# Optimization experiments

Measured on AMD Instinct MI355X. Metric: run time of the kernel, lower is better.

## Reference

```python
import jax, jax.numpy as jnp
import numpy as np

V = 100000   # num_vertices
E = 3200000  # directed edges (symmetric: both directions of E//2 undirected edges)
B = 8        # batch of meshes
C = 3        # xyz vertex features


def setup_inputs() -> dict:
    key = jax.random.key(0)
    k1, k2, k3, k4 = jax.random.split(key, 4)
    src = jax.random.randint(k1, (E // 2,), 0, V, dtype=jnp.int32)
    dst = jax.random.randint(k2, (E // 2,), 0, V, dtype=jnp.int32)
    edge_index = jnp.stack([jnp.concatenate([src, dst]),
                            jnp.concatenate([dst, src])])  # (2, E)
    features = jax.random.normal(k3, (B, V, C), dtype=jnp.float32)
    target_features = jax.random.normal(k4, (B, V, C), dtype=jnp.float32)
    return {"features": features, "target_features": target_features,
            "edge_index": edge_index}


def _sym_laplacian(edge_index, num_nodes, dtype):
    """get_laplacian(..., normalization='sym'): L = I - D^{-1/2} A D^{-1/2}.
    Returns (lap_row, lap_col, lap_weight) as edge list with self-loops appended."""
    row, col = edge_index
    ones = jnp.ones(row.shape, dtype)
    deg = jax.ops.segment_sum(ones, row, num_segments=num_nodes)
    deg_inv_sqrt = jnp.where(deg > 0, deg, 1.0) ** -0.5
    deg_inv_sqrt = jnp.where(deg > 0, deg_inv_sqrt, 0.0)
    ew = -deg_inv_sqrt[row] * deg_inv_sqrt[col]
    loop = jnp.arange(num_nodes, dtype=row.dtype)
    lap_row = jnp.concatenate([row, loop])
    lap_col = jnp.concatenate([col, loop])
    lap_w = jnp.concatenate([ew, jnp.ones((num_nodes,), dtype)])
    return lap_row, lap_col, lap_w


def _apply_laplacian(x, lap_row, lap_col, lap_w, num_nodes):
    # x: (B, V, C) -> gather on source vertex, scale, scatter_add on target vertex
    xt = jnp.swapaxes(x, 0, 1)                       # (V, B, C)
    msg = xt[lap_row] * lap_w[:, None, None]          # (E+V, B, C)
    out = jax.ops.segment_sum(msg, lap_col, num_segments=num_nodes)  # (V, B, C)
    return jnp.swapaxes(out, 0, 1)                    # (B, V, C)


def reference(features, target_features, edge_index):
    lap_row, lap_col, lap_w = _sym_laplacian(edge_index, V, features.dtype)
    lap_x = _apply_laplacian(features, lap_row, lap_col, lap_w, V)
    lap_y = _apply_laplacian(target_features, lap_row, lap_col, lap_w, V)
    # per-batch mse averaged over batch == global mean since shapes are uniform
    return jnp.mean((lap_x - lap_y) ** 2)
```

## Files before the change

### kernel.cpp

```cpp
#include <hip/hip_runtime.h>

#define C_CONST 3
#define B_CONST 8
#define BC 24
#define NCH 3
#define VP 196
#define NP 512
#define CAP 6784
#define K1_T 512
#define K1_EPT 16
#define K1_EPB (K1_T * K1_EPT)
#define PREP_T 512
#define GT 256

typedef float floatx2 __attribute__((ext_vector_type(2)));

__global__ __launch_bounds__(K1_T) void bucket_kernel(
    const int* __restrict__ row, const int* __restrict__ col, int E,
    int* __restrict__ pcount, unsigned int* __restrict__ bucket)
{
    __shared__ unsigned int sl[K1_EPB];
    __shared__ int hist[NP];
    __shared__ int offs[NP];
    __shared__ int gbase[NP];
    __shared__ int scanbuf[NP];
    int tid = threadIdx.x;
    for (int i = tid; i < NP; i += K1_T) hist[i] = 0;
    __syncthreads();

    int e0 = blockIdx.x * K1_EPB + tid * K1_EPT;
    unsigned int pk[K1_EPT];
    int pe[K1_EPT];
    int rk[K1_EPT];
    if (e0 + K1_EPT <= E) {
        int rs[K1_EPT], cs[K1_EPT];
#pragma unroll
        for (int q = 0; q < K1_EPT / 4; q++) {
            int4 rv = *(const int4*)(row + e0 + q * 4);
            int4 cv = *(const int4*)(col + e0 + q * 4);
            rs[q*4+0] = rv.x; rs[q*4+1] = rv.y; rs[q*4+2] = rv.z; rs[q*4+3] = rv.w;
            cs[q*4+0] = cv.x; cs[q*4+1] = cv.y; cs[q*4+2] = cv.z; cs[q*4+3] = cv.w;
        }
#pragma unroll
        for (int i = 0; i < K1_EPT; i++) {
            int c = cs[i];
            int p = c / VP;
            pe[i] = p;
            pk[i] = (unsigned int)rs[i] | ((unsigned int)(c - p * VP) << 17);
        }
    } else {
#pragma unroll
        for (int i = 0; i < K1_EPT; i++) {
            int e = e0 + i;
            if (e < E) {
                int c = col[e];
                int p = c / VP;
                pe[i] = p;
                pk[i] = (unsigned int)row[e] | ((unsigned int)(c - p * VP) << 17);
            } else { pe[i] = -1; pk[i] = 0; }
        }
    }
#pragma unroll
    for (int i = 0; i < K1_EPT; i++)
        rk[i] = (pe[i] >= 0) ? atomicAdd(&hist[pe[i]], 1) : 0;
    __syncthreads();

    scanbuf[tid] = hist[tid];
    __syncthreads();
    for (int off = 1; off < NP; off <<= 1) {
        int t2 = (tid >= off) ? scanbuf[tid - off] : 0;
        __syncthreads();
        scanbuf[tid] += t2;
        __syncthreads();
    }
    offs[tid] = scanbuf[tid] - hist[tid];
    gbase[tid] = (hist[tid] > 0) ? atomicAdd(&pcount[tid], hist[tid]) : 0;
    __syncthreads();

#pragma unroll
    for (int i = 0; i < K1_EPT; i++)
        if (pe[i] >= 0) sl[offs[pe[i]] + rk[i]] = pk[i];
    __syncthreads();

    int wid = tid >> 6, lane = tid & 63;
    for (int pp = wid; pp < NP; pp += K1_T / 64) {
        int cnt = hist[pp];
        int lo = offs[pp];
        int gb = gbase[pp];
        unsigned int* dst = bucket + (size_t)pp * CAP;
        for (int i = lane; i < cnt; i += 64) {
            int pos = gb + i;
            if (pos < CAP) dst[pos] = sl[lo + i];
        }
    }
}

__global__ __launch_bounds__(PREP_T) void prep_sort_kernel(
    const int* __restrict__ pcount, unsigned int* __restrict__ bucket,
    const float* __restrict__ x, const float* __restrict__ y, int V,
    int* __restrict__ rowstart, int* __restrict__ degs,
    unsigned char* __restrict__ wh)
{
    __shared__ unsigned int sorted[CAP];
    __shared__ int rowptr[VP + 1];
    __shared__ int cur[VP];
    __shared__ int scanbuf[256];
    __shared__ float ssc[VP];
    __shared__ unsigned char tile[VP * BC];
    int p = blockIdx.x;
    int tid = threadIdx.x;
    int n = pcount[p]; if (n > CAP) n = CAP;
    unsigned int* bp = bucket + (size_t)p * CAP;

    for (int i = tid; i < VP; i += PREP_T) cur[i] = 0;
    __syncthreads();
    for (int i = tid; i < n; i += PREP_T) atomicAdd(&cur[bp[i] >> 17], 1);
    __syncthreads();

    if (tid < 256) scanbuf[tid] = (tid < VP) ? cur[tid] : 0;
    __syncthreads();
    for (int off = 1; off < 256; off <<= 1) {
        int t2 = 0;
        if (tid < 256 && tid >= off) t2 = scanbuf[tid - off];
        __syncthreads();
        if (tid < 256) scanbuf[tid] += t2;
        __syncthreads();
    }
    if (tid == 0) rowptr[0] = 0;
    if (tid < VP) rowptr[tid + 1] = scanbuf[tid];
    for (int i = tid; i < VP; i += PREP_T) cur[i] = 0;
    __syncthreads();

    for (int i = tid; i < n; i += PREP_T) {
        unsigned int e = bp[i];
        int cl = e >> 17;
        int slot = rowptr[cl] + atomicAdd(&cur[cl], 1);
        sorted[slot] = e & 0x1FFFFu;
    }
    __syncthreads();

    for (int i = tid; i < n; i += PREP_T) bp[i] = sorted[i];

    int vb = p * VP;
    int nv = V - vb; if (nv > VP) nv = VP; if (nv < 0) nv = 0;
    for (int i = tid; i < nv; i += PREP_T) {
        int dg = rowptr[i + 1] - rowptr[i];
        rowstart[vb + i] = p * CAP + rowptr[i];
        degs[vb + i] = dg;
        ssc[i] = (dg > 0) ? rsqrtf((float)dg) : 1.0f;
    }
    __syncthreads();

    int ns = nv * C_CONST;
    int ns4 = ns >> 2;
    for (int idx = tid; idx < B_CONST * ns4; idx += PREP_T) {
        int b = idx / ns4;
        int q = idx - b * ns4;
        size_t off = ((size_t)b * V + vb) * C_CONST + (size_t)q * 4;
        float4 xv = *(const float4*)(x + off);
        float4 yv = *(const float4*)(y + off);
        float vals[4] = {xv.x - yv.x, xv.y - yv.y, xv.z - yv.z, xv.w - yv.w};
        int f0 = q * 4;
#pragma unroll
        for (int j = 0; j < 4; j++) {
            int f = f0 + j;
            int vl = f / C_CONST;
            int c = f - vl * C_CONST;
            float w = ssc[vl] * vals[j];
            int packed = __builtin_amdgcn_cvt_pk_fp8_f32(w, w, 0, false);
            tile[vl * BC + b * C_CONST + c] = (unsigned char)(packed & 0xFF);
        }
    }
    __syncthreads();

    int nbytes = nv * BC;
    uint4* dst = (uint4*)(wh + (size_t)vb * BC);
    const uint4* srcT = (const uint4*)tile;
    for (int i = tid; i < (nbytes >> 4); i += PREP_T) dst[i] = srcT[i];
}

__global__ __launch_bounds__(GT) void gather_loss_kernel(
    const unsigned int* __restrict__ sorted, const int* __restrict__ rowstart,
    const int* __restrict__ degs, const uint2* __restrict__ whp,
    int V, float inv_n, float* __restrict__ out)
{
    __shared__ float ls[GT / 64];
    int item = blockIdx.x * GT + threadIdx.x;
    float s = 0.0f;
    if (item < V * NCH) {
        int v = item / NCH;
        int j = item - v * NCH;
        int q0 = rowstart[v];
        int dg = degs[v];
        float a0=0.f,a1=0.f,a2=0.f,a3=0.f,a4=0.f,a5=0.f,a6=0.f,a7=0.f;
        for (int q = q0; q < q0 + dg; q++) {
            int r = (int)sorted[q];
            uint2 u = whp[r * NCH + j];
            floatx2 f0 = __builtin_amdgcn_cvt_pk_f32_fp8((int)u.x, false);
            floatx2 f1 = __builtin_amdgcn_cvt_pk_f32_fp8((int)u.x, true);
            floatx2 f2 = __builtin_amdgcn_cvt_pk_f32_fp8((int)u.y, false);
            floatx2 f3 = __builtin_amdgcn_cvt_pk_f32_fp8((int)u.y, true);
            a0 += f0.x; a1 += f0.y; a2 += f1.x; a3 += f1.y;
            a4 += f2.x; a5 += f2.y; a6 += f3.x; a7 += f3.y;
        }
        float dvv = (dg > 0) ? rsqrtf((float)dg) : 0.0f;
        float di  = (dg > 0) ? sqrtf((float)dg)  : 1.0f;
        uint2 su = whp[v * NCH + j];
        floatx2 s0 = __builtin_amdgcn_cvt_pk_f32_fp8((int)su.x, false);
        floatx2 s1 = __builtin_amdgcn_cvt_pk_f32_fp8((int)su.x, true);
        floatx2 s2 = __builtin_amdgcn_cvt_pk_f32_fp8((int)su.y, false);
        floatx2 s3 = __builtin_amdgcn_cvt_pk_f32_fp8((int)su.y, true);
        float r0 = s0.x * di - dvv * a0;
        float r1 = s0.y * di - dvv * a1;
        float r2 = s1.x * di - dvv * a2;
        float r3 = s1.y * di - dvv * a3;
        float r4 = s2.x * di - dvv * a4;
        float r5 = s2.y * di - dvv * a5;
        float r6 = s3.x * di - dvv * a6;
        float r7 = s3.y * di - dvv * a7;
        s = r0*r0 + r1*r1 + r2*r2 + r3*r3 + r4*r4 + r5*r5 + r6*r6 + r7*r7;
    }
    for (int off = 32; off > 0; off >>= 1) s += __shfl_down(s, off, 64);
    int lane = threadIdx.x & 63;
    int wid = threadIdx.x >> 6;
    if (lane == 0) ls[wid] = s;
    __syncthreads();
    if (threadIdx.x == 0) {
        float tot = 0.0f;
        for (int i = 0; i < GT / 64; i++) tot += ls[i];
        atomicAdd(out, tot * inv_n);
    }
}

extern "C" void kernel_launch(void* const* d_in, const int* in_sizes, int n_in,
                              void* d_out, int out_size, void* d_ws, size_t ws_size,
                              hipStream_t stream) {
    const float* x = (const float*)d_in[0];
    const float* y = (const float*)d_in[1];
    const int*  ei = (const int*)d_in[2];

    const int E = in_sizes[2] / 2;
    const int V = in_sizes[0] / (B_CONST * C_CONST);
    const int* row = ei;
    const int* col = ei + E;

    char* ws = (char*)d_ws;
    size_t off = 0;
    unsigned int* bucket = (unsigned int*)(ws + off); off += (size_t)NP * CAP * 4;
    unsigned char* wh = (unsigned char*)(ws + off);   off += (size_t)NP * VP * BC;
    int* rowstart = (int*)(ws + off);  off += (size_t)(V + 64) * 4;
    int* degs     = (int*)(ws + off);  off += (size_t)(V + 64) * 4;
    int* pcount   = (int*)(ws + off);  off += (size_t)NP * 4;
    float* outf = (float*)d_out;

    hipMemsetAsync(pcount, 0, (size_t)NP * sizeof(int), stream);
    hipMemsetAsync(d_out, 0, sizeof(float), stream);

    bucket_kernel<<<(E + K1_EPB - 1) / K1_EPB, K1_T, 0, stream>>>(row, col, E, pcount, bucket);
    prep_sort_kernel<<<NP, PREP_T, 0, stream>>>(pcount, bucket, x, y, V, rowstart, degs, wh);
    gather_loss_kernel<<<(V * NCH + GT - 1) / GT, GT, 0, stream>>>(
        bucket, rowstart, degs, (const uint2*)wh, V, 1.0f / (float)(V * BC), outf);
}
```

Before: 166.9 us.

## Make gather kernel process one partition per block with LDS-staged adjacency

The gather/loss kernel now runs one block per vertex partition (NP blocks of 576 threads). Each block copies its sorted neighbor list and per-partition row pointers into shared memory, so it no longer reads per-vertex rowstart/degs and neighbor indices from global memory. The prep kernel writes a per-partition rowptr array in place of those two arrays. The cost is far fewer blocks (512) with large LDS use, which may reduce occupancy and load-balance across CUs, while the irregular fp8 neighbor-feature gathers still come from global memory.

```diff
diff --git a/kernel.cpp b/kernel.cpp
--- a/kernel.cpp
+++ b/kernel.cpp
@@ -11,7 +11,7 @@
 #define K1_EPT 16
 #define K1_EPB (K1_T * K1_EPT)
 #define PREP_T 512
-#define GT 256
+#define GT 576
 
 typedef float floatx2 __attribute__((ext_vector_type(2)));
 
@@ -98,8 +98,7 @@
 __global__ __launch_bounds__(PREP_T) void prep_sort_kernel(
     const int* __restrict__ pcount, unsigned int* __restrict__ bucket,
     const float* __restrict__ x, const float* __restrict__ y, int V,
-    int* __restrict__ rowstart, int* __restrict__ degs,
-    unsigned char* __restrict__ wh)
+    int* __restrict__ rowptr_g, unsigned char* __restrict__ wh)
 {
     __shared__ unsigned int sorted[CAP];
     __shared__ int rowptr[VP + 1];
@@ -140,13 +139,12 @@
     __syncthreads();
 
     for (int i = tid; i < n; i += PREP_T) bp[i] = sorted[i];
+    for (int i = tid; i <= VP; i += PREP_T) rowptr_g[p * (VP + 1) + i] = rowptr[i];
 
     int vb = p * VP;
     int nv = V - vb; if (nv > VP) nv = VP; if (nv < 0) nv = 0;
     for (int i = tid; i < nv; i += PREP_T) {
         int dg = rowptr[i + 1] - rowptr[i];
-        rowstart[vb + i] = p * CAP + rowptr[i];
-        degs[vb + i] = dg;
         ssc[i] = (dg > 0) ? rsqrtf((float)dg) : 1.0f;
     }
     __syncthreads();
@@ -180,52 +178,66 @@
 }
 
 __global__ __launch_bounds__(GT) void gather_loss_kernel(
-    const unsigned int* __restrict__ sorted, const int* __restrict__ rowstart,
-    const int* __restrict__ degs, const uint2* __restrict__ whp,
+    const int* __restrict__ pcount, const unsigned int* __restrict__ sortedg,
+    const int* __restrict__ rowptr_g, const uint2* __restrict__ whp,
     int V, float inv_n, float* __restrict__ out)
 {
+    __shared__ unsigned int sorted[CAP];
+    __shared__ int rowptr[VP + 1];
     __shared__ float ls[GT / 64];
-    int item = blockIdx.x * GT + threadIdx.x;
+    int p = blockIdx.x;
+    int tid = threadIdx.x;
+    int n = pcount[p]; if (n > CAP) n = CAP;
+    const unsigned int* bp = sortedg + (size_t)p * CAP;
+
+    for (int i = tid; i < n; i += GT) sorted[i] = bp[i];
+    for (int i = tid; i <= VP; i += GT) rowptr[i] = rowptr_g[p * (VP + 1) + i];
+    __syncthreads();
+
     float s = 0.0f;
-    if (item < V * NCH) {
-        int v = item / NCH;
-        int j = item - v * NCH;
-        int q0 = rowstart[v];
-        int dg = degs[v];
-        float a0=0.f,a1=0.f,a2=0.f,a3=0.f,a4=0.f,a5=0.f,a6=0.f,a7=0.f;
-        for (int q = q0; q < q0 + dg; q++) {
-            int r = (int)sorted[q];
-            uint2 u = whp[r * NCH + j];
-            floatx2 f0 = __builtin_amdgcn_cvt_pk_f32_fp8((int)u.x, false);
-            floatx2 f1 = __builtin_amdgcn_cvt_pk_f32_fp8((int)u.x, true);
-            floatx2 f2 = __builtin_amdgcn_cvt_pk_f32_fp8((int)u.y, false);
-            floatx2 f3 = __builtin_amdgcn_cvt_pk_f32_fp8((int)u.y, true);
-            a0 += f0.x; a1 += f0.y; a2 += f1.x; a3 += f1.y;
-            a4 += f2.x; a5 += f2.y; a6 += f3.x; a7 += f3.y;
-        }
-        float dvv = (dg > 0) ? rsqrtf((float)dg) : 0.0f;
-        float di  = (dg > 0) ? sqrtf((float)dg)  : 1.0f;
-        uint2 su = whp[v * NCH + j];
-        floatx2 s0 = __builtin_amdgcn_cvt_pk_f32_fp8((int)su.x, false);
-        floatx2 s1 = __builtin_amdgcn_cvt_pk_f32_fp8((int)su.x, true);
-        floatx2 s2 = __builtin_amdgcn_cvt_pk_f32_fp8((int)su.y, false);
-        floatx2 s3 = __builtin_amdgcn_cvt_pk_f32_fp8((int)su.y, true);
-        float r0 = s0.x * di - dvv * a0;
-        float r1 = s0.y * di - dvv * a1;
-        float r2 = s1.x * di - dvv * a2;
-        float r3 = s1.y * di - dvv * a3;
-        float r4 = s2.x * di - dvv * a4;
-        float r5 = s2.y * di - dvv * a5;
-        float r6 = s3.x * di - dvv * a6;
-        float r7 = s3.y * di - dvv * a7;
-        s = r0*r0 + r1*r1 + r2*r2 + r3*r3 + r4*r4 + r5*r5 + r6*r6 + r7*r7;
-    }
+    for (int item = tid; item < VP * NCH; item += GT) {
+        int cl = item / NCH;
+        int j = item - cl * NCH;
+        int v = p * VP + cl;
+        if (v < V) {
+            int q0 = rowptr[cl], q1 = rowptr[cl + 1];
+            int dg = q1 - q0;
+            float a0=0.f,a1=0.f,a2=0.f,a3=0.f,a4=0.f,a5=0.f,a6=0.f,a7=0.f;
+            for (int q = q0; q < q1; q++) {
+                int r = (int)sorted[q];
+                uint2 u = whp[r * NCH + j];
+                floatx2 f0 = __builtin_amdgcn_cvt_pk_f32_fp8((int)u.x, false);
+                floatx2 f1 = __builtin_amdgcn_cvt_pk_f32_fp8((int)u.x, true);
+                floatx2 f2 = __builtin_amdgcn_cvt_pk_f32_fp8((int)u.y, false);
+                floatx2 f3 = __builtin_amdgcn_cvt_pk_f32_fp8((int)u.y, true);
+                a0 += f0.x; a1 += f0.y; a2 += f1.x; a3 += f1.y;
+                a4 += f2.x; a5 += f2.y; a6 += f3.x; a7 += f3.y;
+            }
+            float dvv = (dg > 0) ? rsqrtf((float)dg) : 0.0f;
+            float di  = (dg > 0) ? sqrtf((float)dg)  : 1.0f;
+            uint2 su = whp[v * NCH + j];
+            floatx2 s0 = __builtin_amdgcn_cvt_pk_f32_fp8((int)su.x, false);
+            floatx2 s1 = __builtin_amdgcn_cvt_pk_f32_fp8((int)su.x, true);
+            floatx2 s2 = __builtin_amdgcn_cvt_pk_f32_fp8((int)su.y, false);
+            floatx2 s3 = __builtin_amdgcn_cvt_pk_f32_fp8((int)su.y, true);
+            float r0 = s0.x * di - dvv * a0;
+            float r1 = s0.y * di - dvv * a1;
+            float r2 = s1.x * di - dvv * a2;
+            float r3 = s1.y * di - dvv * a3;
+            float r4 = s2.x * di - dvv * a4;
+            float r5 = s2.y * di - dvv * a5;
+            float r6 = s3.x * di - dvv * a6;
+            float r7 = s3.y * di - dvv * a7;
+            s += r0*r0 + r1*r1 + r2*r2 + r3*r3 + r4*r4 + r5*r5 + r6*r6 + r7*r7;
+        }
+    }
+
     for (int off = 32; off > 0; off >>= 1) s += __shfl_down(s, off, 64);
-    int lane = threadIdx.x & 63;
-    int wid = threadIdx.x >> 6;
+    int lane = tid & 63;
+    int wid = tid >> 6;
     if (lane == 0) ls[wid] = s;
     __syncthreads();
-    if (threadIdx.x == 0) {
+    if (tid == 0) {
         float tot = 0.0f;
         for (int i = 0; i < GT / 64; i++) tot += ls[i];
         atomicAdd(out, tot * inv_n);
@@ -248,8 +260,7 @@
     size_t off = 0;
     unsigned int* bucket = (unsigned int*)(ws + off); off += (size_t)NP * CAP * 4;
     unsigned char* wh = (unsigned char*)(ws + off);   off += (size_t)NP * VP * BC;
-    int* rowstart = (int*)(ws + off);  off += (size_t)(V + 64) * 4;
-    int* degs     = (int*)(ws + off);  off += (size_t)(V + 64) * 4;
+    int* rowptr_g = (int*)(ws + off);  off += (size_t)NP * (VP + 1) * 4;
     int* pcount   = (int*)(ws + off);  off += (size_t)NP * 4;
     float* outf = (float*)d_out;
 
@@ -257,7 +268,8 @@
     hipMemsetAsync(d_out, 0, sizeof(float), stream);
 
     bucket_kernel<<<(E + K1_EPB - 1) / K1_EPB, K1_T, 0, stream>>>(row, col, E, pcount, bucket);
-    prep_sort_kernel<<<NP, PREP_T, 0, stream>>>(pcount, bucket, x, y, V, rowstart, degs, wh);
-    gather_loss_kernel<<<(V * NCH + GT - 1) / GT, GT, 0, stream>>>(
-        bucket, rowstart, degs, (const uint2*)wh, V, 1.0f / (float)(V * BC), outf);
-}
+    prep_sort_kernel<<<NP, PREP_T, 0, stream>>>(pcount, bucket, x, y, V, rowptr_g, wh);
+    gather_loss_kernel<<<NP, GT, 0, stream>>>(pcount, bucket, rowptr_g,
+                                              (const uint2*)wh, V,
+                                              1.0f / (float)(V * BC), outf);
+}
```

After: 151.8 us. 1.1x faster.
